# Optimization experiments

Hardware: AMD Instinct MI355X
Metric: run time of the kernel (lower is better)

Reference implementation:

```python
import jax, jax.numpy as jnp
import numpy as np

N = 100000      # nodes
E = 1600000     # edges (avg degree 16)
IN = 128        # in_feats
H = 4           # num_heads
F = 32          # out_feats per head
NEG_SLOPE = 0.2


def setup_inputs() -> dict:
    key = jax.random.key(0)
    k0, k1, k2, k3, k4, k5 = jax.random.split(key, 6)
    feat = jax.random.normal(k0, (N, IN), dtype=jnp.float32)
    # Glorot-ish scaled params
    W = jax.random.normal(k1, (IN, H * F), dtype=jnp.float32) * (1.0 / np.sqrt(IN))
    attn_l = jax.random.normal(k2, (H, F), dtype=jnp.float32) * 0.1
    attn_r = jax.random.normal(k3, (H, F), dtype=jnp.float32) * 0.1
    bias = jnp.zeros((H * F,), dtype=jnp.float32)
    src = jax.random.randint(k4, (E,), 0, N, dtype=jnp.int32)
    dst = jax.random.randint(k5, (E,), 0, N, dtype=jnp.int32)
    return {"feat": feat, "W": W, "attn_l": attn_l, "attn_r": attn_r,
            "bias": bias, "src": src, "dst": dst}


def reference(feat, W, attn_l, attn_r, bias, src, dst):
    # GeMM: projected features, [N, H, F]
    feat_src = (feat @ W).reshape(N, H, F)
    # per-node attention halves, [N, H]
    el = (feat_src * attn_l).sum(-1)
    er = (feat_src * attn_r).sum(-1)
    # per-edge score e_ij = LeakyReLU(el[src] + er[dst]), [E, H]
    e = el[src] + er[dst]
    e = jnp.where(e > 0, e, NEG_SLOPE * e)
    # edge softmax over destination-node segments (numerically stable)
    m = jax.ops.segment_max(e, dst, num_segments=N)          # [N, H]
    ex = jnp.exp(e - m[dst])                                  # [E, H]
    denom = jax.ops.segment_sum(ex, dst, num_segments=N)     # [N, H]
    alpha = ex / jnp.maximum(denom[dst], 1e-9)                # [E, H]
    # weighted SpMM aggregation: sum_j alpha_ij * Wh_j, [N, H, F]
    msg = feat_src[src] * alpha[:, :, None]                   # [E, H, F]
    rst = jax.ops.segment_sum(msg, dst, num_segments=N)      # [N, H, F]
    rst = rst + bias.reshape(1, H, F)
    return rst
```

## Files before the change

kernel.cpp:

```cpp
#include <hip/hip_runtime.h>
#include <hip/hip_fp16.h>

#define IN_F 128
#define HF   128
#define NH   4
#define NF   32

#define NPB       256
#define NPB_SHIFT 8
#define BIN_CHUNK 4096
#define HIST_BLOCKS 256
#define WFRAG_BLOCKS 8

typedef __attribute__((ext_vector_type(8))) short short8v;
typedef __attribute__((ext_vector_type(4))) float f32x4;

__device__ __forceinline__ unsigned short f32_to_bf16_rtn(float f) {
    unsigned int u = __float_as_uint(f);
    u += 0x7fffu + ((u >> 16) & 1u);
    return (unsigned short)(u >> 16);
}

#define FMA_MIX_LO(acc, pair, w) \
    asm("v_fma_mix_f32 %0, %1, %2, %0 op_sel:[0,0,0] op_sel_hi:[1,0,0]" \
        : "+v"(acc) : "v"(pair), "v"(w))
#define FMA_MIX_HI(acc, pair, w) \
    asm("v_fma_mix_f32 %0, %1, %2, %0 op_sel:[1,0,0] op_sel_hi:[1,0,0]" \
        : "+v"(acc) : "v"(pair), "v"(w))

__device__ __forceinline__ void gemm_body(
    int row0b, char* smem,
    const float* __restrict__ feat, const short8v* __restrict__ wfrag,
    const float* __restrict__ attn_l, const float* __restrict__ attn_r,
    unsigned short* __restrict__ feat_src_h,
    float* __restrict__ el, float* __restrict__ er, int N, int t) {
    unsigned short* a_lds = (unsigned short*)smem;
    unsigned short* w_lds = (unsigned short*)(smem + 16384);
    const int lane = t & 63;
    const int wave = t >> 6;

    {
        const uint4* wsrc = (const uint4*)wfrag;
        uint4* wdst = (uint4*)w_lds;
        #pragma unroll
        for (int i = 0; i < 8; ++i)
            wdst[i * 256 + t] = wsrc[i * 256 + t];
    }
    #pragma unroll
    for (int i = 0; i < 8; ++i) {
        int idx = i * 256 + t;
        int row = idx >> 5;
        int c4  = idx & 31;
        int srow = min(row0b + row, N - 1);
        float4 f = *(const float4*)(feat + (size_t)srow * IN_F + c4 * 4);
        unsigned int lo = ((unsigned int)f32_to_bf16_rtn(f.y) << 16) | f32_to_bf16_rtn(f.x);
        unsigned int hi = ((unsigned int)f32_to_bf16_rtn(f.w) << 16) | f32_to_bf16_rtn(f.z);
        int kb = c4 >> 3, g = (c4 >> 1) & 3, half = c4 & 1;
        int wv = row >> 4, m = row & 15;
        unsigned int* p = (unsigned int*)a_lds;
        int u = (wv * 4096 + kb * 1024 + g * 256 + m * 16 + half * 8) >> 2;
        p[u]     = lo;
        p[u + 1] = hi;
    }
    __syncthreads();

    const int m = lane & 15;
    const int g = lane >> 4;
    short8v aw[4];
    #pragma unroll
    for (int kb = 0; kb < 4; ++kb)
        aw[kb] = *(const short8v*)&a_lds[wave * 2048 + kb * 512 + g * 128 + m * 8];

    f32x4 acc[8];
    #pragma unroll
    for (int nt = 0; nt < 8; ++nt) acc[nt] = (f32x4){0.f, 0.f, 0.f, 0.f};

    #pragma unroll
    for (int nt = 0; nt < 8; ++nt) {
        #pragma unroll
        for (int kb = 0; kb < 4; ++kb) {
            short8v bw = *(const short8v*)&w_lds[((nt * 4 + kb) * 64 + lane) * 8];
            acc[nt] = __builtin_amdgcn_mfma_f32_16x16x32_bf16(aw[kb], bw, acc[nt], 0, 0, 0);
        }
    }

    float al[8], ar[8];
    #pragma unroll
    for (int nt = 0; nt < 8; ++nt) {
        al[nt] = attn_l[nt * 16 + m];
        ar[nt] = attn_r[nt * 16 + m];
    }

    #pragma unroll
    for (int r = 0; r < 4; ++r) {
        const int row = row0b + wave * 16 + 4 * g + r;
        const bool valid = (row < N);
        if (valid) {
            #pragma unroll
            for (int nt = 0; nt < 8; ++nt)
                feat_src_h[(size_t)row * HF + nt * 16 + m] =
                    __half_as_ushort(__float2half(acc[nt][r]));
        }
        float pl[NH], pr[NH];
        #pragma unroll
        for (int h = 0; h < NH; ++h) {
            pl[h] = acc[2 * h][r] * al[2 * h] + acc[2 * h + 1][r] * al[2 * h + 1];
            pr[h] = acc[2 * h][r] * ar[2 * h] + acc[2 * h + 1][r] * ar[2 * h + 1];
        }
        #pragma unroll
        for (int mask = 1; mask <= 8; mask <<= 1) {
            #pragma unroll
            for (int h = 0; h < NH; ++h) {
                pl[h] += __shfl_xor(pl[h], mask);
                pr[h] += __shfl_xor(pr[h], mask);
            }
        }
        if (valid && m == 0) {
            *(float4*)(el + (size_t)row * NH) = make_float4(pl[0], pl[1], pl[2], pl[3]);
            *(float4*)(er + (size_t)row * NH) = make_float4(pr[0], pr[1], pr[2], pr[3]);
        }
    }
}

__global__ void __launch_bounds__(256)
gat_wfrag_hist(const float* __restrict__ W, short8v* __restrict__ wfrag,
               const int* __restrict__ dst, int* __restrict__ bcount,
               int E, int nbuck, int chunk) {
    const int t = threadIdx.x;
    if ((int)blockIdx.x < WFRAG_BLOCKS) {
        const int entry = blockIdx.x * 256 + t;
        const int lane = entry & 63;
        const int kb   = (entry >> 6) & 3;
        const int nt   = entry >> 8;
        const int k0   = kb * 32 + (lane >> 4) * 8;
        const int col  = nt * 16 + (lane & 15);
        short8v s;
        #pragma unroll
        for (int j = 0; j < 8; ++j)
            s[j] = (short)f32_to_bf16_rtn(W[(k0 + j) * HF + col]);
        wfrag[entry] = s;
        return;
    }
    __shared__ int h[512];
    for (int i = t; i < 512; i += 256) h[i] = 0;
    __syncthreads();
    const int hb = blockIdx.x - WFRAG_BLOCKS;
    const int e0 = hb * chunk;
    const int e1 = min(e0 + chunk, E);
    for (int e = e0 + t; e < e1; e += 256)
        atomicAdd(&h[dst[e] >> NPB_SHIFT], 1);
    __syncthreads();
    for (int b = t; b < nbuck; b += 256)
        if (h[b]) atomicAdd(&bcount[b], h[b]);
}

__global__ void __launch_bounds__(512)
gat_bucket_scan(const int* __restrict__ bcount, int* __restrict__ bbase,
                int* __restrict__ gcursor, int* __restrict__ offsets,
                int N, int E, int nbuck) {
    __shared__ int buf[512];
    const int t = threadIdx.x;
    int v = (t < nbuck) ? bcount[t] : 0;
    buf[t] = v;
    __syncthreads();
    for (int off = 1; off < 512; off <<= 1) {
        int x = (t >= off) ? buf[t - off] : 0;
        __syncthreads();
        buf[t] += x;
        __syncthreads();
    }
    if (t < nbuck) {
        int base = buf[t] - v;
        bbase[t]   = base;
        gcursor[t] = base;
    }
    if (t == 0) {
        bbase[nbuck] = E;
        offsets[N]   = E;
    }
}

__global__ void __launch_bounds__(256)
gat_bin_gemm(const int* __restrict__ src, const int* __restrict__ dst,
             int* __restrict__ gcursor, unsigned int* __restrict__ gpairs, int E,
             int nBin,
             const float* __restrict__ feat, const short8v* __restrict__ wfrag,
             const float* __restrict__ attn_l, const float* __restrict__ attn_r,
             unsigned short* __restrict__ feat_src_h,
             float* __restrict__ el, float* __restrict__ er, int N) {
    __shared__ __align__(16) char smem[49152];
    const int t = threadIdx.x;

    if ((int)blockIdx.x < nBin) {
        unsigned int*   stage  = (unsigned int*)smem;
        unsigned short* buckof = (unsigned short*)(smem + 16384);
        int* hist  = (int*)(smem + 24576);
        int* sc    = (int*)(smem + 26624);
        int* basew = (int*)(smem + 28672);
        int* cur   = (int*)(smem + 30720);
        for (int i = t; i < 512; i += 256) hist[i] = 0;
        __syncthreads();
        const int e0  = blockIdx.x * BIN_CHUNK;
        const int cnt = min(BIN_CHUNK, E - e0);
        for (int i = t; i < cnt; i += 256)
            atomicAdd(&hist[dst[e0 + i] >> NPB_SHIFT], 1);
        __syncthreads();
        sc[t]       = hist[t];
        sc[t + 256] = hist[t + 256];
        __syncthreads();
        for (int off = 1; off < 512; off <<= 1) {
            int x0 = (t >= off) ? sc[t - off] : 0;
            int x1 = sc[t + 256 - off];
            __syncthreads();
            sc[t]       += x0;
            sc[t + 256] += x1;
            __syncthreads();
        }
        for (int b = t; b < 512; b += 256) {
            int c  = hist[b];
            int ex = sc[b] - c;
            cur[b] = ex;
            basew[b] = c ? atomicAdd(&gcursor[b], c) : 0;
        }
        __syncthreads();
        for (int i = t; i < cnt; i += 256) {
            unsigned s = (unsigned)src[e0 + i];
            unsigned d = (unsigned)dst[e0 + i];
            int b = (int)(d >> NPB_SHIFT);
            int p = atomicAdd(&cur[b], 1);
            stage[p]  = (s << 8) | (d & (NPB - 1));
            buckof[p] = (unsigned short)b;
        }
        __syncthreads();
        for (int j = t; j < cnt; j += 256) {
            int b  = (int)buckof[j];
            int ex = sc[b] - hist[b];
            gpairs[basew[b] + (j - ex)] = stage[j];
        }
        return;
    }

    gemm_body((blockIdx.x - nBin) * 64, smem, feat, wfrag, attn_l, attn_r,
              feat_src_h, el, er, N, t);
}

__global__ void __launch_bounds__(256)
gat_fine_gemm(const unsigned int* __restrict__ gpairs, const int* __restrict__ bbase,
              int* __restrict__ offsets, int* __restrict__ slot, int nFine, int gemmA,
              const float* __restrict__ feat, const short8v* __restrict__ wfrag,
              const float* __restrict__ attn_l, const float* __restrict__ attn_r,
              unsigned short* __restrict__ feat_src_h,
              float* __restrict__ el, float* __restrict__ er, int N) {
    __shared__ __align__(16) char smem[49152];
    const int t = threadIdx.x;

    if ((int)blockIdx.x < nFine) {
        int* h   = (int*)smem;
        int* buf = (int*)(smem + 1024);
        int* cur = (int*)(smem + 2048);
        const int b     = blockIdx.x;
        const int node0 = b << NPB_SHIFT;
        const int beg = bbase[b];
        const int end = bbase[b + 1];
        h[t] = 0;
        __syncthreads();
        for (int i = beg + t; i < end; i += 256)
            atomicAdd(&h[gpairs[i] & (NPB - 1)], 1);
        __syncthreads();
        int v = h[t];
        buf[t] = v;
        __syncthreads();
        for (int off = 1; off < 256; off <<= 1) {
            int x = (t >= off) ? buf[t - off] : 0;
            __syncthreads();
            buf[t] += x;
            __syncthreads();
        }
        int ex = buf[t] - v;
        if (node0 + t < N) offsets[node0 + t] = beg + ex;
        cur[t] = ex;
        __syncthreads();
        for (int i = beg + t; i < end; i += 256) {
            unsigned pr = gpairs[i];
            int p = atomicAdd(&cur[pr & (NPB - 1)], 1);
            slot[beg + p] = (int)(pr >> 8);
        }
        return;
    }

    gemm_body((gemmA + (int)blockIdx.x - nFine) * 64, smem, feat, wfrag,
              attn_l, attn_r, feat_src_h, el, er, N, t);
}

__global__ void __launch_bounds__(256)
gat_aggregate(const unsigned short* __restrict__ feat_src_h,
              const float* __restrict__ el, const float* __restrict__ er,
              const int* __restrict__ offsets, const int* __restrict__ slot,
              const float* __restrict__ bias, float* __restrict__ out, int N) {
    __shared__ int   ss[4][64];
    __shared__ float exs[4][256];
    const int lane = threadIdx.x & 63;
    const int wave = threadIdx.x >> 6;
    const int node = blockIdx.x * 4 + wave;
    if (node >= N) return;
    const int start = offsets[node];
    const int end   = offsets[node + 1];
    const int k  = lane & 15;
    const int g  = lane >> 4;
    const int hm = k >> 2;

    const float4 er4 = *(const float4*)(er + (size_t)node * NH);
    float dacc = 0.f;
    float ax0 = 0.f, ax1 = 0.f, ax2 = 0.f, ax3 = 0.f;
    float ax4 = 0.f, ax5 = 0.f, ax6 = 0.f, ax7 = 0.f;
    const unsigned short* fsp = feat_src_h + 8 * k;
    int*   ssw = ss[wave];
    float* exw = exs[wave];

    for (int c = start; c < end; c += 64) {
        int idx = c + lane;
        bool vld = idx < end;
        int s_l = vld ? slot[idx] : 0;
        float4 ev = make_float4(0.f, 0.f, 0.f, 0.f);
        if (vld) ev = *(const float4*)(el + (size_t)s_l * NH);
        float x0 = ev.x + er4.x; x0 = fmaxf(x0, 0.2f * x0);
        float x1 = ev.y + er4.y; x1 = fmaxf(x1, 0.2f * x1);
        float x2 = ev.z + er4.z; x2 = fmaxf(x2, 0.2f * x2);
        float x3 = ev.w + er4.w; x3 = fmaxf(x3, 0.2f * x3);
        float e0 = vld ? __expf(x0) : 0.f;
        float e1 = vld ? __expf(x1) : 0.f;
        float e2 = vld ? __expf(x2) : 0.f;
        float e3 = vld ? __expf(x3) : 0.f;
        ssw[lane] = s_l;
        *(float4*)&exw[lane * 4] = make_float4(e0, e1, e2, e3);
        asm volatile("" ::: "memory");
        const int n = min(64, end - c);
        int j = g;
        for (; j + 4 < n; j += 8) {
            int jB = j + 4;
            int sA = ssw[j];
            int sB = ssw[jB];
            float wA = exw[j * 4 + hm];
            float wB = exw[jB * 4 + hm];
            uint4 uA = *(const uint4*)(fsp + (size_t)sA * HF);
            uint4 uB = *(const uint4*)(fsp + (size_t)sB * HF);
            dacc += wA + wB;
            FMA_MIX_LO(ax0, uA.x, wA); FMA_MIX_LO(ax0, uB.x, wB);
            FMA_MIX_HI(ax1, uA.x, wA); FMA_MIX_HI(ax1, uB.x, wB);
            FMA_MIX_LO(ax2, uA.y, wA); FMA_MIX_LO(ax2, uB.y, wB);
            FMA_MIX_HI(ax3, uA.y, wA); FMA_MIX_HI(ax3, uB.y, wB);
            FMA_MIX_LO(ax4, uA.z, wA); FMA_MIX_LO(ax4, uB.z, wB);
            FMA_MIX_HI(ax5, uA.z, wA); FMA_MIX_HI(ax5, uB.z, wB);
            FMA_MIX_LO(ax6, uA.w, wA); FMA_MIX_LO(ax6, uB.w, wB);
            FMA_MIX_HI(ax7, uA.w, wA); FMA_MIX_HI(ax7, uB.w, wB);
        }
        if (j < n) {
            int sA = ssw[j];
            float wA = exw[j * 4 + hm];
            uint4 uA = *(const uint4*)(fsp + (size_t)sA * HF);
            dacc += wA;
            FMA_MIX_LO(ax0, uA.x, wA);
            FMA_MIX_HI(ax1, uA.x, wA);
            FMA_MIX_LO(ax2, uA.y, wA);
            FMA_MIX_HI(ax3, uA.y, wA);
            FMA_MIX_LO(ax4, uA.z, wA);
            FMA_MIX_HI(ax5, uA.z, wA);
            FMA_MIX_LO(ax6, uA.w, wA);
            FMA_MIX_HI(ax7, uA.w, wA);
        }
        asm volatile("" ::: "memory");
    }

    #pragma unroll
    for (int msk = 16; msk <= 32; msk <<= 1) {
        ax0 += __shfl_xor(ax0, msk); ax1 += __shfl_xor(ax1, msk);
        ax2 += __shfl_xor(ax2, msk); ax3 += __shfl_xor(ax3, msk);
        ax4 += __shfl_xor(ax4, msk); ax5 += __shfl_xor(ax5, msk);
        ax6 += __shfl_xor(ax6, msk); ax7 += __shfl_xor(ax7, msk);
        dacc += __shfl_xor(dacc, msk);
    }
    const float inv = 1.0f / fmaxf(dacc, 1e-9f);

    if (g == 0) {
        float4 b0 = *(const float4*)(bias + 8 * k);
        float4 b1 = *(const float4*)(bias + 8 * k + 4);
        float4 o0, o1;
        o0.x = ax0 * inv + b0.x; o0.y = ax1 * inv + b0.y;
        o0.z = ax2 * inv + b0.z; o0.w = ax3 * inv + b0.w;
        o1.x = ax4 * inv + b1.x; o1.y = ax5 * inv + b1.y;
        o1.z = ax6 * inv + b1.z; o1.w = ax7 * inv + b1.w;
        *(float4*)(out + (size_t)node * HF + 8 * k)     = o0;
        *(float4*)(out + (size_t)node * HF + 8 * k + 4) = o1;
    }
}

extern "C" void kernel_launch(void* const* d_in, const int* in_sizes, int n_in,
                              void* d_out, int out_size, void* d_ws, size_t ws_size,
                              hipStream_t stream) {
    const float* feat   = (const float*)d_in[0];
    const float* W      = (const float*)d_in[1];
    const float* attn_l = (const float*)d_in[2];
    const float* attn_r = (const float*)d_in[3];
    const float* bias   = (const float*)d_in[4];
    const int*   src    = (const int*)d_in[5];
    const int*   dst    = (const int*)d_in[6];
    float* out = (float*)d_out;

    const int N = in_sizes[0] / IN_F;
    const int E = in_sizes[5];
    const int nbuck = (N + NPB - 1) / NPB;

    char* ws = (char*)d_ws;
    size_t off = 0;
    auto alloc = [&](size_t bytes) -> void* {
        off = (off + 255) & ~(size_t)255;
        void* p = ws + off;
        off += bytes;
        return p;
    };
    unsigned short* feat_src_h = (unsigned short*)alloc((size_t)N * HF * sizeof(unsigned short));
    float* el      = (float*)alloc((size_t)N * NH * sizeof(float));
    float* er      = (float*)alloc((size_t)N * NH * sizeof(float));
    int*   bcount  = (int*)  alloc((size_t)(nbuck + 1) * sizeof(int));
    int*   bbase   = (int*)  alloc((size_t)(nbuck + 1) * sizeof(int));
    int*   gcursor = (int*)  alloc((size_t)nbuck * sizeof(int));
    int*   offsets = (int*)  alloc((size_t)(N + 1) * sizeof(int));
    unsigned int* gpairs = (unsigned int*)alloc((size_t)E * sizeof(unsigned int));
    int*   slot    = (int*)  alloc((size_t)E * sizeof(int));
    short8v* wfrag = (short8v*)alloc((size_t)2048 * sizeof(short8v));

    hipMemsetAsync(bcount, 0, (size_t)(nbuck + 1) * sizeof(int), stream);

    const int chunk1 = (E + HIST_BLOCKS - 1) / HIST_BLOCKS;
    gat_wfrag_hist<<<WFRAG_BLOCKS + HIST_BLOCKS, 256, 0, stream>>>(
        W, wfrag, dst, bcount, E, nbuck, chunk1);

    gat_bucket_scan<<<1, 512, 0, stream>>>(bcount, bbase, gcursor, offsets, N, E, nbuck);

    const int nBin = (E + BIN_CHUNK - 1) / BIN_CHUNK;
    const int gemmBlocks = (N + 63) / 64;
    const int gemmA = (gemmBlocks * 3) / 5;
    const int gemmB = gemmBlocks - gemmA;
    gat_bin_gemm<<<nBin + gemmA, 256, 0, stream>>>(
        src, dst, gcursor, gpairs, E, nBin,
        feat, wfrag, attn_l, attn_r, feat_src_h, el, er, N);

    gat_fine_gemm<<<nbuck + gemmB, 256, 0, stream>>>(
        gpairs, bbase, offsets, slot, nbuck, gemmA,
        feat, wfrag, attn_l, attn_r, feat_src_h, el, er, N);

    gat_aggregate<<<(N + 3) / 4, 256, 0, stream>>>(feat_src_h, el, er, offsets, slot, bias, out, N);
}
```

Measured before the change: 141.6 us.

## Fuse fine-grained CSR build into aggregation using shared-memory slot lists per node quarter

Replaces the separate fine-sort kernel, which wrote global offsets and slot arrays, and the aggregate kernel with a single kernel. Each block takes a quarter of a 256-node bucket, reads the bucket's pairs into registers, builds a per-node histogram, scan and slot list in LDS, then aggregates 64 nodes across 4 waves. All GEMM blocks move into the binning launch. This removes a kernel launch and the global slot and offset round-trip, but each bucket's pairs are now read four times. Buckets are capped at RP*256 pairs, so an unusually dense bucket would be silently truncated.

```diff
diff --git a/kernel.cpp b/kernel.cpp
--- a/kernel.cpp
+++ b/kernel.cpp
@@ -11,6 +11,8 @@
 #define BIN_CHUNK 4096
 #define HIST_BLOCKS 256
 #define WFRAG_BLOCKS 8
+#define QCAP 1536
+#define RP   18
 
 typedef __attribute__((ext_vector_type(8))) short short8v;
 typedef __attribute__((ext_vector_type(4))) float f32x4;
@@ -156,8 +158,7 @@
 
 __global__ void __launch_bounds__(512)
 gat_bucket_scan(const int* __restrict__ bcount, int* __restrict__ bbase,
-                int* __restrict__ gcursor, int* __restrict__ offsets,
-                int N, int E, int nbuck) {
+                int* __restrict__ gcursor, int E, int nbuck) {
     __shared__ int buf[512];
     const int t = threadIdx.x;
     int v = (t < nbuck) ? bcount[t] : 0;
@@ -174,10 +175,7 @@
         bbase[t]   = base;
         gcursor[t] = base;
     }
-    if (t == 0) {
-        bbase[nbuck] = E;
-        offsets[N]   = E;
-    }
+    if (t == 0) bbase[nbuck] = E;
 }
 
 __global__ void __launch_bounds__(256)
@@ -245,152 +243,163 @@
 }
 
 __global__ void __launch_bounds__(256)
-gat_fine_gemm(const unsigned int* __restrict__ gpairs, const int* __restrict__ bbase,
-              int* __restrict__ offsets, int* __restrict__ slot, int nFine, int gemmA,
-              const float* __restrict__ feat, const short8v* __restrict__ wfrag,
-              const float* __restrict__ attn_l, const float* __restrict__ attn_r,
-              unsigned short* __restrict__ feat_src_h,
-              float* __restrict__ el, float* __restrict__ er, int N) {
-    __shared__ __align__(16) char smem[49152];
+gat_fine_agg(const unsigned int* __restrict__ gpairs, const int* __restrict__ bbase,
+             const unsigned short* __restrict__ feat_src_h,
+             const float* __restrict__ el, const float* __restrict__ er,
+             const float* __restrict__ bias, float* __restrict__ out, int N) {
+    __shared__ int   slot_lds[QCAP];
+    __shared__ int   hist[64];
+    __shared__ int   sbuf[64];
+    __shared__ int   offs[65];
+    __shared__ int   cur[64];
+    __shared__ float exs[4][256];
     const int t = threadIdx.x;
-
-    if ((int)blockIdx.x < nFine) {
-        int* h   = (int*)smem;
-        int* buf = (int*)(smem + 1024);
-        int* cur = (int*)(smem + 2048);
-        const int b     = blockIdx.x;
-        const int node0 = b << NPB_SHIFT;
-        const int beg = bbase[b];
-        const int end = bbase[b + 1];
-        h[t] = 0;
-        __syncthreads();
-        for (int i = beg + t; i < end; i += 256)
-            atomicAdd(&h[gpairs[i] & (NPB - 1)], 1);
-        __syncthreads();
-        int v = h[t];
-        buf[t] = v;
-        __syncthreads();
-        for (int off = 1; off < 256; off <<= 1) {
-            int x = (t >= off) ? buf[t - off] : 0;
-            __syncthreads();
-            buf[t] += x;
-            __syncthreads();
-        }
-        int ex = buf[t] - v;
-        if (node0 + t < N) offsets[node0 + t] = beg + ex;
-        cur[t] = ex;
-        __syncthreads();
-        for (int i = beg + t; i < end; i += 256) {
-            unsigned pr = gpairs[i];
-            int p = atomicAdd(&cur[pr & (NPB - 1)], 1);
-            slot[beg + p] = (int)(pr >> 8);
-        }
-        return;
-    }
-
-    gemm_body((gemmA + (int)blockIdx.x - nFine) * 64, smem, feat, wfrag,
-              attn_l, attn_r, feat_src_h, el, er, N, t);
-}
-
-__global__ void __launch_bounds__(256)
-gat_aggregate(const unsigned short* __restrict__ feat_src_h,
-              const float* __restrict__ el, const float* __restrict__ er,
-              const int* __restrict__ offsets, const int* __restrict__ slot,
-              const float* __restrict__ bias, float* __restrict__ out, int N) {
-    __shared__ int   ss[4][64];
-    __shared__ float exs[4][256];
-    const int lane = threadIdx.x & 63;
-    const int wave = threadIdx.x >> 6;
-    const int node = blockIdx.x * 4 + wave;
-    if (node >= N) return;
-    const int start = offsets[node];
-    const int end   = offsets[node + 1];
+    const int b = blockIdx.x >> 2;
+    const int q = blockIdx.x & 3;
+    const int node0 = (b << NPB_SHIFT) + q * 64;
+    const int beg = bbase[b];
+    const int end = bbase[b + 1];
+
+    if (t < 64) hist[t] = 0;
+    __syncthreads();
+
+    unsigned int pv[RP];
+    #pragma unroll
+    for (int r = 0; r < RP; ++r) {
+        int idx = beg + r * 256 + t;
+        pv[r] = 0xffffffffu;
+        if (idx < end) {
+            unsigned int pr = gpairs[idx];
+            pv[r] = pr;
+            int local = (int)(pr & (NPB - 1)) - q * 64;
+            if (local >= 0 && local < 64) atomicAdd(&hist[local], 1);
+        }
+    }
+    __syncthreads();
+    if (t < 64) sbuf[t] = hist[t];
+    __syncthreads();
+    for (int off = 1; off < 64; off <<= 1) {
+        int x = (t < 64 && t >= off) ? sbuf[t - off] : 0;
+        __syncthreads();
+        if (t < 64) sbuf[t] += x;
+        __syncthreads();
+    }
+    if (t < 64) {
+        offs[t + 1] = sbuf[t];
+        cur[t] = sbuf[t] - hist[t];
+        if (t == 0) offs[0] = 0;
+    }
+    __syncthreads();
+    #pragma unroll
+    for (int r = 0; r < RP; ++r) {
+        unsigned int pr = pv[r];
+        if (pr != 0xffffffffu) {
+            int local = (int)(pr & (NPB - 1)) - q * 64;
+            if (local >= 0 && local < 64) {
+                int p = atomicAdd(&cur[local], 1);
+                slot_lds[p] = (int)(pr >> 8);
+            }
+        }
+    }
+    __syncthreads();
+
+    const int lane = t & 63;
+    const int wave = t >> 6;
     const int k  = lane & 15;
     const int g  = lane >> 4;
     const int hm = k >> 2;
-
-    const float4 er4 = *(const float4*)(er + (size_t)node * NH);
-    float dacc = 0.f;
-    float ax0 = 0.f, ax1 = 0.f, ax2 = 0.f, ax3 = 0.f;
-    float ax4 = 0.f, ax5 = 0.f, ax6 = 0.f, ax7 = 0.f;
     const unsigned short* fsp = feat_src_h + 8 * k;
-    int*   ssw = ss[wave];
     float* exw = exs[wave];
-
-    for (int c = start; c < end; c += 64) {
-        int idx = c + lane;
-        bool vld = idx < end;
-        int s_l = vld ? slot[idx] : 0;
-        float4 ev = make_float4(0.f, 0.f, 0.f, 0.f);
-        if (vld) ev = *(const float4*)(el + (size_t)s_l * NH);
-        float x0 = ev.x + er4.x; x0 = fmaxf(x0, 0.2f * x0);
-        float x1 = ev.y + er4.y; x1 = fmaxf(x1, 0.2f * x1);
-        float x2 = ev.z + er4.z; x2 = fmaxf(x2, 0.2f * x2);
-        float x3 = ev.w + er4.w; x3 = fmaxf(x3, 0.2f * x3);
-        float e0 = vld ? __expf(x0) : 0.f;
-        float e1 = vld ? __expf(x1) : 0.f;
-        float e2 = vld ? __expf(x2) : 0.f;
-        float e3 = vld ? __expf(x3) : 0.f;
-        ssw[lane] = s_l;
-        *(float4*)&exw[lane * 4] = make_float4(e0, e1, e2, e3);
-        asm volatile("" ::: "memory");
-        const int n = min(64, end - c);
-        int j = g;
-        for (; j + 4 < n; j += 8) {
-            int jB = j + 4;
-            int sA = ssw[j];
-            int sB = ssw[jB];
-            float wA = exw[j * 4 + hm];
-            float wB = exw[jB * 4 + hm];
-            uint4 uA = *(const uint4*)(fsp + (size_t)sA * HF);
-            uint4 uB = *(const uint4*)(fsp + (size_t)sB * HF);
-            dacc += wA + wB;
-            FMA_MIX_LO(ax0, uA.x, wA); FMA_MIX_LO(ax0, uB.x, wB);
-            FMA_MIX_HI(ax1, uA.x, wA); FMA_MIX_HI(ax1, uB.x, wB);
-            FMA_MIX_LO(ax2, uA.y, wA); FMA_MIX_LO(ax2, uB.y, wB);
-            FMA_MIX_HI(ax3, uA.y, wA); FMA_MIX_HI(ax3, uB.y, wB);
-            FMA_MIX_LO(ax4, uA.z, wA); FMA_MIX_LO(ax4, uB.z, wB);
-            FMA_MIX_HI(ax5, uA.z, wA); FMA_MIX_HI(ax5, uB.z, wB);
-            FMA_MIX_LO(ax6, uA.w, wA); FMA_MIX_LO(ax6, uB.w, wB);
-            FMA_MIX_HI(ax7, uA.w, wA); FMA_MIX_HI(ax7, uB.w, wB);
-        }
-        if (j < n) {
-            int sA = ssw[j];
-            float wA = exw[j * 4 + hm];
-            uint4 uA = *(const uint4*)(fsp + (size_t)sA * HF);
-            dacc += wA;
-            FMA_MIX_LO(ax0, uA.x, wA);
-            FMA_MIX_HI(ax1, uA.x, wA);
-            FMA_MIX_LO(ax2, uA.y, wA);
-            FMA_MIX_HI(ax3, uA.y, wA);
-            FMA_MIX_LO(ax4, uA.z, wA);
-            FMA_MIX_HI(ax5, uA.z, wA);
-            FMA_MIX_LO(ax6, uA.w, wA);
-            FMA_MIX_HI(ax7, uA.w, wA);
-        }
-        asm volatile("" ::: "memory");
-    }
-
-    #pragma unroll
-    for (int msk = 16; msk <= 32; msk <<= 1) {
-        ax0 += __shfl_xor(ax0, msk); ax1 += __shfl_xor(ax1, msk);
-        ax2 += __shfl_xor(ax2, msk); ax3 += __shfl_xor(ax3, msk);
-        ax4 += __shfl_xor(ax4, msk); ax5 += __shfl_xor(ax5, msk);
-        ax6 += __shfl_xor(ax6, msk); ax7 += __shfl_xor(ax7, msk);
-        dacc += __shfl_xor(dacc, msk);
-    }
-    const float inv = 1.0f / fmaxf(dacc, 1e-9f);
-
+    float4 b0, b1;
     if (g == 0) {
-        float4 b0 = *(const float4*)(bias + 8 * k);
-        float4 b1 = *(const float4*)(bias + 8 * k + 4);
-        float4 o0, o1;
-        o0.x = ax0 * inv + b0.x; o0.y = ax1 * inv + b0.y;
-        o0.z = ax2 * inv + b0.z; o0.w = ax3 * inv + b0.w;
-        o1.x = ax4 * inv + b1.x; o1.y = ax5 * inv + b1.y;
-        o1.z = ax6 * inv + b1.z; o1.w = ax7 * inv + b1.w;
-        *(float4*)(out + (size_t)node * HF + 8 * k)     = o0;
-        *(float4*)(out + (size_t)node * HF + 8 * k + 4) = o1;
+        b0 = *(const float4*)(bias + 8 * k);
+        b1 = *(const float4*)(bias + 8 * k + 4);
+    }
+
+    for (int i = 0; i < 16; ++i) {
+        const int l = wave + 4 * i;
+        const int node = node0 + l;
+        if (node >= N) break;
+        const int s0 = offs[l];
+        const int s1 = offs[l + 1];
+
+        const float4 er4 = *(const float4*)(er + (size_t)node * NH);
+        float dacc = 0.f;
+        float ax0 = 0.f, ax1 = 0.f, ax2 = 0.f, ax3 = 0.f;
+        float ax4 = 0.f, ax5 = 0.f, ax6 = 0.f, ax7 = 0.f;
+
+        for (int c = s0; c < s1; c += 64) {
+            int idx = c + lane;
+            bool vld = idx < s1;
+            int s_l = vld ? slot_lds[idx] : 0;
+            float4 ev = make_float4(0.f, 0.f, 0.f, 0.f);
+            if (vld) ev = *(const float4*)(el + (size_t)s_l * NH);
+            float x0 = ev.x + er4.x; x0 = fmaxf(x0, 0.2f * x0);
+            float x1 = ev.y + er4.y; x1 = fmaxf(x1, 0.2f * x1);
+            float x2 = ev.z + er4.z; x2 = fmaxf(x2, 0.2f * x2);
+            float x3 = ev.w + er4.w; x3 = fmaxf(x3, 0.2f * x3);
+            float e0 = vld ? __expf(x0) : 0.f;
+            float e1 = vld ? __expf(x1) : 0.f;
+            float e2 = vld ? __expf(x2) : 0.f;
+            float e3 = vld ? __expf(x3) : 0.f;
+            *(float4*)&exw[lane * 4] = make_float4(e0, e1, e2, e3);
+            asm volatile("" ::: "memory");
+            const int n = min(64, s1 - c);
+            int j = g;
+            for (; j + 4 < n; j += 8) {
+                int jB = j + 4;
+                int sA = slot_lds[c + j];
+                int sB = slot_lds[c + jB];
+                float wA = exw[j * 4 + hm];
+                float wB = exw[jB * 4 + hm];
+                uint4 uA = *(const uint4*)(fsp + (size_t)sA * HF);
+                uint4 uB = *(const uint4*)(fsp + (size_t)sB * HF);
+                dacc += wA + wB;
+                FMA_MIX_LO(ax0, uA.x, wA); FMA_MIX_LO(ax0, uB.x, wB);
+                FMA_MIX_HI(ax1, uA.x, wA); FMA_MIX_HI(ax1, uB.x, wB);
+                FMA_MIX_LO(ax2, uA.y, wA); FMA_MIX_LO(ax2, uB.y, wB);
+                FMA_MIX_HI(ax3, uA.y, wA); FMA_MIX_HI(ax3, uB.y, wB);
+                FMA_MIX_LO(ax4, uA.z, wA); FMA_MIX_LO(ax4, uB.z, wB);
+                FMA_MIX_HI(ax5, uA.z, wA); FMA_MIX_HI(ax5, uB.z, wB);
+                FMA_MIX_LO(ax6, uA.w, wA); FMA_MIX_LO(ax6, uB.w, wB);
+                FMA_MIX_HI(ax7, uA.w, wA); FMA_MIX_HI(ax7, uB.w, wB);
+            }
+            if (j < n) {
+                int sA = slot_lds[c + j];
+                float wA = exw[j * 4 + hm];
+                uint4 uA = *(const uint4*)(fsp + (size_t)sA * HF);
+                dacc += wA;
+                FMA_MIX_LO(ax0, uA.x, wA);
+                FMA_MIX_HI(ax1, uA.x, wA);
+                FMA_MIX_LO(ax2, uA.y, wA);
+                FMA_MIX_HI(ax3, uA.y, wA);
+                FMA_MIX_LO(ax4, uA.z, wA);
+                FMA_MIX_HI(ax5, uA.z, wA);
+                FMA_MIX_LO(ax6, uA.w, wA);
+                FMA_MIX_HI(ax7, uA.w, wA);
+            }
+            asm volatile("" ::: "memory");
+        }
+
+        #pragma unroll
+        for (int msk = 16; msk <= 32; msk <<= 1) {
+            ax0 += __shfl_xor(ax0, msk); ax1 += __shfl_xor(ax1, msk);
+            ax2 += __shfl_xor(ax2, msk); ax3 += __shfl_xor(ax3, msk);
+            ax4 += __shfl_xor(ax4, msk); ax5 += __shfl_xor(ax5, msk);
+            ax6 += __shfl_xor(ax6, msk); ax7 += __shfl_xor(ax7, msk);
+            dacc += __shfl_xor(dacc, msk);
+        }
+        const float inv = 1.0f / fmaxf(dacc, 1e-9f);
+
+        if (g == 0) {
+            float4 o0, o1;
+            o0.x = ax0 * inv + b0.x; o0.y = ax1 * inv + b0.y;
+            o0.z = ax2 * inv + b0.z; o0.w = ax3 * inv + b0.w;
+            o1.x = ax4 * inv + b1.x; o1.y = ax5 * inv + b1.y;
+            o1.z = ax6 * inv + b1.z; o1.w = ax7 * inv + b1.w;
+            *(float4*)(out + (size_t)node * HF + 8 * k)     = o0;
+            *(float4*)(out + (size_t)node * HF + 8 * k + 4) = o1;
+        }
     }
 }
 
@@ -424,9 +433,7 @@
     int*   bcount  = (int*)  alloc((size_t)(nbuck + 1) * sizeof(int));
     int*   bbase   = (int*)  alloc((size_t)(nbuck + 1) * sizeof(int));
     int*   gcursor = (int*)  alloc((size_t)nbuck * sizeof(int));
-    int*   offsets = (int*)  alloc((size_t)(N + 1) * sizeof(int));
     unsigned int* gpairs = (unsigned int*)alloc((size_t)E * sizeof(unsigned int));
-    int*   slot    = (int*)  alloc((size_t)E * sizeof(int));
     short8v* wfrag = (short8v*)alloc((size_t)2048 * sizeof(short8v));
 
     hipMemsetAsync(bcount, 0, (size_t)(nbuck + 1) * sizeof(int), stream);
@@ -435,19 +442,14 @@
     gat_wfrag_hist<<<WFRAG_BLOCKS + HIST_BLOCKS, 256, 0, stream>>>(
         W, wfrag, dst, bcount, E, nbuck, chunk1);
 
-    gat_bucket_scan<<<1, 512, 0, stream>>>(bcount, bbase, gcursor, offsets, N, E, nbuck);
+    gat_bucket_scan<<<1, 512, 0, stream>>>(bcount, bbase, gcursor, E, nbuck);
 
     const int nBin = (E + BIN_CHUNK - 1) / BIN_CHUNK;
     const int gemmBlocks = (N + 63) / 64;
-    const int gemmA = (gemmBlocks * 3) / 5;
-    const int gemmB = gemmBlocks - gemmA;
-    gat_bin_gemm<<<nBin + gemmA, 256, 0, stream>>>(
+    gat_bin_gemm<<<nBin + gemmBlocks, 256, 0, stream>>>(
         src, dst, gcursor, gpairs, E, nBin,
         feat, wfrag, attn_l, attn_r, feat_src_h, el, er, N);
 
-    gat_fine_gemm<<<nbuck + gemmB, 256, 0, stream>>>(
-        gpairs, bbase, offsets, slot, nbuck, gemmA,
-        feat, wfrag, attn_l, attn_r, feat_src_h, el, er, N);
-
-    gat_aggregate<<<(N + 3) / 4, 256, 0, stream>>>(feat_src_h, el, er, offsets, slot, bias, out, N);
-}
+    gat_fine_agg<<<nbuck * 4, 256, 0, stream>>>(
+        gpairs, bbase, feat_src_h, el, er, bias, out, N);
+}
```

New measurement: 139.7 us. Within noise of the previous version (-1.4%).

## Slice aggregation by feature columns so each block reads a narrow column band

Applied to the files above, without the earlier changes.

Replaces the one-wave-per-node aggregation with a kernel that splits the 128 output features into 8 slices of 16 columns. Each block handles one slice for a chunk of 64 nodes, with each wave processing 4 nodes at once and 16 edges per node per step. The aim is a smaller working set per block in the gathered feature table, for better L2/cache locality, and less padding waste on low-degree nodes. In exchange, slot and el are re-read and exp is recomputed 8 times, and the gathers shrink to 16-byte segments per row.

```diff
diff --git a/kernel.cpp b/kernel.cpp
--- a/kernel.cpp
+++ b/kernel.cpp
@@ -11,6 +11,7 @@
 #define BIN_CHUNK 4096
 #define HIST_BLOCKS 256
 #define WFRAG_BLOCKS 8
+#define NPW 16
 
 typedef __attribute__((ext_vector_type(8))) short short8v;
 typedef __attribute__((ext_vector_type(4))) float f32x4;
@@ -293,104 +294,101 @@
 }
 
 __global__ void __launch_bounds__(256)
-gat_aggregate(const unsigned short* __restrict__ feat_src_h,
-              const float* __restrict__ el, const float* __restrict__ er,
-              const int* __restrict__ offsets, const int* __restrict__ slot,
-              const float* __restrict__ bias, float* __restrict__ out, int N) {
+gat_agg_sliced(const unsigned short* __restrict__ feat_src_h,
+               const float* __restrict__ el, const float* __restrict__ er,
+               const int* __restrict__ offsets, const int* __restrict__ slot,
+               const float* __restrict__ bias, float* __restrict__ out, int N) {
     __shared__ int   ss[4][64];
-    __shared__ float exs[4][256];
-    const int lane = threadIdx.x & 63;
-    const int wave = threadIdx.x >> 6;
-    const int node = blockIdx.x * 4 + wave;
-    if (node >= N) return;
-    const int start = offsets[node];
-    const int end   = offsets[node + 1];
-    const int k  = lane & 15;
-    const int g  = lane >> 4;
-    const int hm = k >> 2;
-
-    const float4 er4 = *(const float4*)(er + (size_t)node * NH);
-    float dacc = 0.f;
-    float ax0 = 0.f, ax1 = 0.f, ax2 = 0.f, ax3 = 0.f;
-    float ax4 = 0.f, ax5 = 0.f, ax6 = 0.f, ax7 = 0.f;
-    const unsigned short* fsp = feat_src_h + 8 * k;
+    __shared__ float exs[4][64];
+    const int t = threadIdx.x;
+    const int lane = t & 63;
+    const int wave = t >> 6;
+    const int slice = blockIdx.x & 7;
+    const int chunk = blockIdx.x >> 3;
+    const int h    = slice >> 1;
+    const int nsub = lane >> 4;
+    const int l16  = lane & 15;
+    const int eidx = l16 >> 1;
+    const int cc   = l16 & 1;
+    const unsigned short* fsp = feat_src_h + slice * 16 + cc * 8;
     int*   ssw = ss[wave];
     float* exw = exs[wave];
 
-    for (int c = start; c < end; c += 64) {
-        int idx = c + lane;
-        bool vld = idx < end;
-        int s_l = vld ? slot[idx] : 0;
-        float4 ev = make_float4(0.f, 0.f, 0.f, 0.f);
-        if (vld) ev = *(const float4*)(el + (size_t)s_l * NH);
-        float x0 = ev.x + er4.x; x0 = fmaxf(x0, 0.2f * x0);
-        float x1 = ev.y + er4.y; x1 = fmaxf(x1, 0.2f * x1);
-        float x2 = ev.z + er4.z; x2 = fmaxf(x2, 0.2f * x2);
-        float x3 = ev.w + er4.w; x3 = fmaxf(x3, 0.2f * x3);
-        float e0 = vld ? __expf(x0) : 0.f;
-        float e1 = vld ? __expf(x1) : 0.f;
-        float e2 = vld ? __expf(x2) : 0.f;
-        float e3 = vld ? __expf(x3) : 0.f;
-        ssw[lane] = s_l;
-        *(float4*)&exw[lane * 4] = make_float4(e0, e1, e2, e3);
-        asm volatile("" ::: "memory");
-        const int n = min(64, end - c);
-        int j = g;
-        for (; j + 4 < n; j += 8) {
-            int jB = j + 4;
-            int sA = ssw[j];
-            int sB = ssw[jB];
-            float wA = exw[j * 4 + hm];
-            float wB = exw[jB * 4 + hm];
-            uint4 uA = *(const uint4*)(fsp + (size_t)sA * HF);
-            uint4 uB = *(const uint4*)(fsp + (size_t)sB * HF);
-            dacc += wA + wB;
-            FMA_MIX_LO(ax0, uA.x, wA); FMA_MIX_LO(ax0, uB.x, wB);
-            FMA_MIX_HI(ax1, uA.x, wA); FMA_MIX_HI(ax1, uB.x, wB);
-            FMA_MIX_LO(ax2, uA.y, wA); FMA_MIX_LO(ax2, uB.y, wB);
-            FMA_MIX_HI(ax3, uA.y, wA); FMA_MIX_HI(ax3, uB.y, wB);
-            FMA_MIX_LO(ax4, uA.z, wA); FMA_MIX_LO(ax4, uB.z, wB);
-            FMA_MIX_HI(ax5, uA.z, wA); FMA_MIX_HI(ax5, uB.z, wB);
-            FMA_MIX_LO(ax6, uA.w, wA); FMA_MIX_LO(ax6, uB.w, wB);
-            FMA_MIX_HI(ax7, uA.w, wA); FMA_MIX_HI(ax7, uB.w, wB);
-        }
-        if (j < n) {
-            int sA = ssw[j];
-            float wA = exw[j * 4 + hm];
-            uint4 uA = *(const uint4*)(fsp + (size_t)sA * HF);
-            dacc += wA;
-            FMA_MIX_LO(ax0, uA.x, wA);
-            FMA_MIX_HI(ax1, uA.x, wA);
-            FMA_MIX_LO(ax2, uA.y, wA);
-            FMA_MIX_HI(ax3, uA.y, wA);
-            FMA_MIX_LO(ax4, uA.z, wA);
-            FMA_MIX_HI(ax5, uA.z, wA);
-            FMA_MIX_LO(ax6, uA.w, wA);
-            FMA_MIX_HI(ax7, uA.w, wA);
-        }
-        asm volatile("" ::: "memory");
-    }
-
-    #pragma unroll
-    for (int msk = 16; msk <= 32; msk <<= 1) {
-        ax0 += __shfl_xor(ax0, msk); ax1 += __shfl_xor(ax1, msk);
-        ax2 += __shfl_xor(ax2, msk); ax3 += __shfl_xor(ax3, msk);
-        ax4 += __shfl_xor(ax4, msk); ax5 += __shfl_xor(ax5, msk);
-        ax6 += __shfl_xor(ax6, msk); ax7 += __shfl_xor(ax7, msk);
-        dacc += __shfl_xor(dacc, msk);
-    }
-    const float inv = 1.0f / fmaxf(dacc, 1e-9f);
-
-    if (g == 0) {
-        float4 b0 = *(const float4*)(bias + 8 * k);
-        float4 b1 = *(const float4*)(bias + 8 * k + 4);
-        float4 o0, o1;
-        o0.x = ax0 * inv + b0.x; o0.y = ax1 * inv + b0.y;
-        o0.z = ax2 * inv + b0.z; o0.w = ax3 * inv + b0.w;
-        o1.x = ax4 * inv + b1.x; o1.y = ax5 * inv + b1.y;
-        o1.z = ax6 * inv + b1.z; o1.w = ax7 * inv + b1.w;
-        *(float4*)(out + (size_t)node * HF + 8 * k)     = o0;
-        *(float4*)(out + (size_t)node * HF + 8 * k + 4) = o1;
+    const float4 b0 = *(const float4*)(bias + slice * 16 + cc * 8);
+    const float4 b1 = *(const float4*)(bias + slice * 16 + cc * 8 + 4);
+
+    const int base = (chunk * 4 + wave) * NPW;
+
+    for (int i = 0; i < NPW; i += 4) {
+        const int node = base + i + nsub;
+        const bool active = node < N;
+        const int nodec = active ? node : N - 1;
+        const int s0 = offsets[nodec];
+        const int s1 = offsets[nodec + 1];
+        const int deg = active ? (s1 - s0) : 0;
+        const float er_h = er[(size_t)nodec * NH + h];
+
+        int nmax = deg;
+        nmax = max(nmax, __shfl_xor(nmax, 16));
+        nmax = max(nmax, __shfl_xor(nmax, 32));
+        const int nch = (nmax + 15) >> 4;
+
+        float dacc = 0.f;
+        float ax0=0.f, ax1=0.f, ax2=0.f, ax3=0.f, ax4=0.f, ax5=0.f, ax6=0.f, ax7=0.f;
+
+        for (int ch = 0; ch < nch; ++ch) {
+            const int off = ch * 16;
+            const bool vld = (off + l16) < deg;
+            int s_l = vld ? slot[s0 + off + l16] : 0;
+            float ev = vld ? el[(size_t)s_l * NH + h] : 0.f;
+            float x = ev + er_h; x = fmaxf(x, 0.2f * x);
+            float e = vld ? __expf(x) : 0.f;
+            ssw[lane] = s_l;
+            exw[lane] = e;
+            asm volatile("" ::: "memory");
+            const int nrem = deg - off;
+            #pragma unroll
+            for (int it = 0; it < 2; ++it) {
+                const int jl = it * 8 + eidx;
+                if (jl < nrem) {
+                    const int j = nsub * 16 + jl;
+                    int sA = ssw[j];
+                    float wA = exw[j];
+                    dacc += wA;
+                    uint4 uA = *(const uint4*)(fsp + (size_t)sA * HF);
+                    FMA_MIX_LO(ax0, uA.x, wA);
+                    FMA_MIX_HI(ax1, uA.x, wA);
+                    FMA_MIX_LO(ax2, uA.y, wA);
+                    FMA_MIX_HI(ax3, uA.y, wA);
+                    FMA_MIX_LO(ax4, uA.z, wA);
+                    FMA_MIX_HI(ax5, uA.z, wA);
+                    FMA_MIX_LO(ax6, uA.w, wA);
+                    FMA_MIX_HI(ax7, uA.w, wA);
+                }
+            }
+            asm volatile("" ::: "memory");
+        }
+
+        #pragma unroll
+        for (int msk = 2; msk <= 8; msk <<= 1) {
+            ax0 += __shfl_xor(ax0, msk); ax1 += __shfl_xor(ax1, msk);
+            ax2 += __shfl_xor(ax2, msk); ax3 += __shfl_xor(ax3, msk);
+            ax4 += __shfl_xor(ax4, msk); ax5 += __shfl_xor(ax5, msk);
+            ax6 += __shfl_xor(ax6, msk); ax7 += __shfl_xor(ax7, msk);
+            dacc += __shfl_xor(dacc, msk);
+        }
+        const float inv = 1.0f / fmaxf(dacc, 1e-9f);
+
+        if (eidx == 0 && active) {
+            float4 o0, o1;
+            o0.x = ax0 * inv + b0.x; o0.y = ax1 * inv + b0.y;
+            o0.z = ax2 * inv + b0.z; o0.w = ax3 * inv + b0.w;
+            o1.x = ax4 * inv + b1.x; o1.y = ax5 * inv + b1.y;
+            o1.z = ax6 * inv + b1.z; o1.w = ax7 * inv + b1.w;
+            float* op = out + (size_t)node * HF + slice * 16 + cc * 8;
+            *(float4*)op       = o0;
+            *(float4*)(op + 4) = o1;
+        }
     }
 }
 
@@ -449,5 +447,7 @@
         gpairs, bbase, offsets, slot, nbuck, gemmA,
         feat, wfrag, attn_l, attn_r, feat_src_h, el, er, N);
 
-    gat_aggregate<<<(N + 3) / 4, 256, 0, stream>>>(feat_src_h, el, er, offsets, slot, bias, out, N);
-}
+    const int aggChunks = (N + 4 * NPW - 1) / (4 * NPW);
+    gat_agg_sliced<<<aggChunks * 8, 256, 0, stream>>>(
+        feat_src_h, el, er, offsets, slot, bias, out, N);
+}
```

Result: slower. 322.9 us (+128.0%).
